# Optimization experiments

Hardware: AMD Instinct MI355X
Metric: run time of the kernel (lower is better)

The kernel has to match this reference:

```python
import jax, jax.numpy as jnp
import numpy as np

N_NODES = 50000
N_EDGES = 400000
IN_C, HID, EDGE_D = 128, 256, 32
NUM_LAYERS = 3

def _gnblock(x, src, dst, edge_attr, ew, eb, nw, nb):
    # edge message MLP: relu(W [x_src, x_dst, e] + b)  -> [E, HID]
    m = jax.nn.relu(jnp.concatenate([x[src], x[dst], edge_attr], axis=-1) @ ew + eb)
    # mean aggregation by destination node
    agg = jax.ops.segment_sum(m, dst, num_segments=N_NODES)
    deg = jax.ops.segment_sum(jnp.ones((m.shape[0],), m.dtype), dst, num_segments=N_NODES)
    agg = agg / jnp.maximum(deg, 1.0)[:, None]
    # node update MLP: relu(W [x, agg] + b) -> [N, HID]
    return jax.nn.relu(jnp.concatenate([x, agg], axis=-1) @ nw + nb)

def setup_inputs() -> dict:
    key = jax.random.key(0)
    ks = jax.random.split(key, 12)
    s = 0.05  # keep activations sane
    return {
        'x': jax.random.normal(ks[0], (N_NODES, IN_C), jnp.float32),
        'edge_index': jax.random.randint(ks[1], (2, N_EDGES), 0, N_NODES, jnp.int32),
        'edge_attr': jax.random.normal(ks[2], (N_EDGES, EDGE_D), jnp.float32),
        'e0_w': jax.random.normal(ks[3], (2 * IN_C + EDGE_D, HID), jnp.float32) * s,
        'e0_b': jnp.zeros((HID,), jnp.float32),
        'n0_w': jax.random.normal(ks[4], (IN_C + HID, HID), jnp.float32) * s,
        'n0_b': jnp.zeros((HID,), jnp.float32),
        'e_w': jax.random.normal(ks[5], (NUM_LAYERS - 1, 2 * HID + EDGE_D, HID), jnp.float32) * s,
        'e_b': jnp.zeros((NUM_LAYERS - 1, HID), jnp.float32),
        'n_w': jax.random.normal(ks[6], (NUM_LAYERS - 1, 2 * HID, HID), jnp.float32) * s,
        'n_b': jnp.zeros((NUM_LAYERS - 1, HID), jnp.float32),
        'h1_w': jax.random.normal(ks[7], (HID, HID), jnp.float32) * s,
        'h1_b': jnp.zeros((HID,), jnp.float32),
        'h2_w': jax.random.normal(ks[8], (HID, 1), jnp.float32) * s,
        'h2_b': jnp.zeros((1,), jnp.float32),
    }

def reference(x, edge_index, edge_attr, e0_w, e0_b, n0_w, n0_b,
              e_w, e_b, n_w, n_b, h1_w, h1_b, h2_w, h2_b):
    src, dst = edge_index[0], edge_index[1]
    h = _gnblock(x, src, dst, edge_attr, e0_w, e0_b, n0_w, n0_b)
    for i in range(NUM_LAYERS - 1):
        h = _gnblock(h, src, dst, edge_attr, e_w[i], e_b[i], n_w[i], n_b[i])
    # MLP head -> per-node logit [N, 1]
    h = jax.nn.relu(h @ h1_w + h1_b)
    return h @ h2_w + h2_b
```

## Files before the change

### kernel.cpp

```cpp
#include <hip/hip_runtime.h>
#include <hip/hip_bf16.h>
#include <hip/hip_fp16.h>

#define NN 50000
#define NE 400000
#define NBLK 196

typedef unsigned short u16;
typedef unsigned int u32;
typedef __attribute__((ext_vector_type(8))) short short8;
typedef __attribute__((ext_vector_type(4))) float f32x4;
typedef __attribute__((ext_vector_type(4))) unsigned short u16x4;
typedef __attribute__((ext_vector_type(2))) _Float16 h2;

typedef __attribute__((address_space(1))) const void as1_void;
typedef __attribute__((address_space(3))) void as3_void;

static __device__ __forceinline__ float bf2f(u16 u) {
    return __uint_as_float(((u32)u) << 16);
}
static __device__ __forceinline__ u16 f2bf(float f) {
    u32 x = __float_as_uint(f);
    x += 0x7fffu + ((x >> 16) & 1u);
    return (u16)(x >> 16);
}
static __device__ __forceinline__ u32 packh2(float a, float b) {
    return ((u32)__half_as_ushort(__float2half(b)) << 16) |
           (u32)__half_as_ushort(__float2half(a));
}
static __device__ __forceinline__ float fdot2u(u32 a, u32 b, float c) {
    return __builtin_amdgcn_fdot2(__builtin_bit_cast(h2, a),
                                  __builtin_bit_cast(h2, b), c, false);
}

static __device__ __forceinline__ void gload_lds16(const u16* g, u16* l) {
    __builtin_amdgcn_global_load_lds((as1_void*)g, (as3_void*)l, 16, 0, 0);
}

__global__ __launch_bounds__(256) void gemm_bt(
    const u16* __restrict__ A, int lda,
    const u16* __restrict__ Bt,
    u16* __restrict__ C, int ldc,
    int M, int K,
    const float* __restrict__ bias,
    int relu)
{
    __shared__ u16 As[128 * 32];
    __shared__ u16 Bs[128 * 32];

    const int t = threadIdx.x;
    const int w = t >> 6;
    const int lane = t & 63;
    const int quad = lane >> 4;
    const int l15 = lane & 15;
    const int tile_m = blockIdx.x * 128;
    const int tile_n = blockIdx.y * 128;
    const int wm = (w >> 1) * 64;
    const int wn = (w & 1) * 64;

    f32x4 acc[4][4];
#pragma unroll
    for (int r = 0; r < 4; ++r)
#pragma unroll
        for (int c = 0; c < 4; ++c)
            acc[r][c] = (f32x4){0.f, 0.f, 0.f, 0.f};

    int ar0 = tile_m + (t >> 2);      if (ar0 > M - 1) ar0 = M - 1;
    int ar1 = tile_m + 64 + (t >> 2); if (ar1 > M - 1) ar1 = M - 1;
    const int br0 = tile_n + (t >> 2);
    const int br1 = tile_n + 64 + (t >> 2);
    const int koff = (t & 3) * 8;

    u16* lAs0 = As + w * 512;
    u16* lAs1 = As + 2048 + w * 512;
    u16* lBs0 = Bs + w * 512;
    u16* lBs1 = Bs + 2048 + w * 512;

    const u16* Arow0 = A + (size_t)ar0 * lda + koff;
    const u16* Arow1 = A + (size_t)ar1 * lda + koff;
    const u16* Brow0 = Bt + (size_t)br0 * K + koff;
    const u16* Brow1 = Bt + (size_t)br1 * K + koff;

    for (int k0 = 0; k0 < K; k0 += 32) {
        gload_lds16(Arow0 + k0, lAs0);
        gload_lds16(Arow1 + k0, lAs1);
        gload_lds16(Brow0 + k0, lBs0);
        gload_lds16(Brow1 + k0, lBs1);
        __syncthreads();

        short8 af[4], bfr[4];
#pragma unroll
        for (int r = 0; r < 4; ++r)
            af[r] = *(const short8*)&As[(wm + r * 16 + l15) * 32 + quad * 8];
#pragma unroll
        for (int c = 0; c < 4; ++c)
            bfr[c] = *(const short8*)&Bs[(wn + c * 16 + l15) * 32 + quad * 8];
#pragma unroll
        for (int r = 0; r < 4; ++r)
#pragma unroll
            for (int c = 0; c < 4; ++c)
                acc[r][c] = __builtin_amdgcn_mfma_f32_16x16x32_bf16(af[r], bfr[c], acc[r][c], 0, 0, 0);
        __syncthreads();
    }

#pragma unroll
    for (int r = 0; r < 4; ++r) {
#pragma unroll
        for (int c = 0; c < 4; ++c) {
            const int coln = tile_n + wn + c * 16 + l15;
            const float bv = bias ? bias[coln] : 0.0f;
#pragma unroll
            for (int i = 0; i < 4; ++i) {
                const int row = tile_m + wm + r * 16 + quad * 4 + i;
                if (row < M) {
                    float v = acc[r][c][i] + bv;
                    if (relu) v = fmaxf(v, 0.f);
                    C[(size_t)row * ldc + coln] = f2bf(v);
                }
            }
        }
    }
}

__global__ __launch_bounds__(256) void edge_agg_fused(
    const u16* __restrict__ P,
    const u32* __restrict__ eattr_p32,
    const u32* __restrict__ WePk,
    const int* __restrict__ row_start,
    const int* __restrict__ src_perm,
    const float* __restrict__ inv_deg,
    u16* __restrict__ aggZ)
{
    const int node = (int)((blockIdx.x * 256 + threadIdx.x) >> 6);
    const int lane = threadIdx.x & 63;
    const int l15 = lane & 15;
    const int col = lane * 4;
    if (node >= NN) return;

    uint4 wpk[16];
#pragma unroll
    for (int kp = 0; kp < 16; ++kp)
        wpk[kp] = *(const uint4*)(WePk + kp * 256 + col);

    u16x4 pdv = *(const u16x4*)(P + (size_t)node * 512 + 256 + col);
    f32x4 pb;
    pb[0] = bf2f(pdv[0]);
    pb[1] = bf2f(pdv[1]);
    pb[2] = bf2f(pdv[2]);
    pb[3] = bf2f(pdv[3]);

    f32x4 accv = (f32x4){0.f, 0.f, 0.f, 0.f};
    const int s0r = row_start[node], s1r = row_start[node + 1];

    if (s1r > s0r) {
        const int jlast = s1r - 1;
        int j1 = (s0r + 1 < jlast) ? s0r + 1 : jlast;
        int sa = src_perm[s0r];
        int sb = src_perm[j1];
        u16x4 psa = *(const u16x4*)(P + (size_t)sa * 512 + col);
        u16x4 psb = *(const u16x4*)(P + (size_t)sb * 512 + col);
        u32 eva = eattr_p32[(size_t)s0r * 16 + l15];
        u32 evb = eattr_p32[(size_t)j1 * 16 + l15];

        for (int j = s0r; j < s1r; ++j) {
            int jc = (j + 2 < jlast) ? j + 2 : jlast;
            int sn = src_perm[jc];
            u16x4 psn = *(const u16x4*)(P + (size_t)sn * 512 + col);
            u32 evn = eattr_p32[(size_t)jc * 16 + l15];

            f32x4 q = pb;
#pragma unroll
            for (int kp = 0; kp < 16; ++kp) {
                u32 evk = (u32)__builtin_amdgcn_readlane((int)eva, kp);
                q[0] = fdot2u(evk, wpk[kp].x, q[0]);
                q[1] = fdot2u(evk, wpk[kp].y, q[1]);
                q[2] = fdot2u(evk, wpk[kp].z, q[2]);
                q[3] = fdot2u(evk, wpk[kp].w, q[3]);
            }
            q[0] += bf2f(psa[0]);
            q[1] += bf2f(psa[1]);
            q[2] += bf2f(psa[2]);
            q[3] += bf2f(psa[3]);
            accv[0] += fmaxf(q[0], 0.f);
            accv[1] += fmaxf(q[1], 0.f);
            accv[2] += fmaxf(q[2], 0.f);
            accv[3] += fmaxf(q[3], 0.f);

            psa = psb; eva = evb;
            psb = psn; evb = evn;
        }
    }

    const float idg = inv_deg[node];
    u16x4 o;
    o[0] = f2bf(accv[0] * idg);
    o[1] = f2bf(accv[1] * idg);
    o[2] = f2bf(accv[2] * idg);
    o[3] = f2bf(accv[3] * idg);
    *(u16x4*)(aggZ + (size_t)node * 512 + col) = o;
}

__global__ __launch_bounds__(256) void head_out(
    const u16* __restrict__ h4Z,
    const float* __restrict__ h2w,
    const float* __restrict__ h2b,
    float* __restrict__ out)
{
    const int node = (int)((blockIdx.x * 256 + threadIdx.x) >> 6);
    const int lane = threadIdx.x & 63;
    if (node >= NN) return;
    const int col = lane * 4;
    u16x4 hv = *(const u16x4*)(h4Z + (size_t)node * 512 + col);
    float4 wv = *(const float4*)(h2w + col);
    float s = bf2f(hv[0]) * wv.x + bf2f(hv[1]) * wv.y +
              bf2f(hv[2]) * wv.z + bf2f(hv[3]) * wv.w;
    for (int off = 32; off > 0; off >>= 1)
        s += __shfl_down(s, off, 64);
    if (lane == 0) out[node] = s + h2b[0];
}

__global__ void zero_int(int* p, int n) {
    int i = blockIdx.x * 256 + threadIdx.x;
    if (i < n) p[i] = 0;
}

__global__ void hist_k(const int* __restrict__ ei, int* __restrict__ deg) {
    int e = blockIdx.x * 256 + threadIdx.x;
    if (e < NE) atomicAdd(&deg[ei[NE + e]], 1);
}

__global__ __launch_bounds__(256) void block_sum_k(const int* __restrict__ deg,
                                                   int* __restrict__ bsum) {
    __shared__ int sm[4];
    const int i = blockIdx.x * 256 + threadIdx.x;
    int v = (i < NN) ? deg[i] : 0;
    for (int off = 32; off > 0; off >>= 1)
        v += __shfl_down(v, off, 64);
    const int lane = threadIdx.x & 63;
    const int w = threadIdx.x >> 6;
    if (lane == 0) sm[w] = v;
    __syncthreads();
    if (threadIdx.x == 0)
        bsum[blockIdx.x] = sm[0] + sm[1] + sm[2] + sm[3];
}

__global__ __launch_bounds__(256) void scan_block_k(const int* __restrict__ bsum,
                                                    int* __restrict__ boff,
                                                    int* __restrict__ row_start) {
    __shared__ int sm[256];
    const int tid = threadIdx.x;
    int v = (tid < NBLK) ? bsum[tid] : 0;
    sm[tid] = v;
    __syncthreads();
    for (int o = 1; o < 256; o <<= 1) {
        int tv = (tid >= o) ? sm[tid - o] : 0;
        __syncthreads();
        sm[tid] += tv;
        __syncthreads();
    }
    if (tid < NBLK) boff[tid] = sm[tid] - v;
    if (tid == NBLK - 1) row_start[NN] = sm[tid];
}

__global__ __launch_bounds__(256) void writeback_k(const int* __restrict__ deg,
                                                   const int* __restrict__ boff,
                                                   int* __restrict__ row_start,
                                                   int* __restrict__ cursor,
                                                   float* __restrict__ inv_deg) {
    __shared__ int sm[256];
    const int tid = threadIdx.x;
    const int i = blockIdx.x * 256 + tid;
    int v = (i < NN) ? deg[i] : 0;
    sm[tid] = v;
    __syncthreads();
    for (int o = 1; o < 256; o <<= 1) {
        int tv = (tid >= o) ? sm[tid - o] : 0;
        __syncthreads();
        sm[tid] += tv;
        __syncthreads();
    }
    if (i < NN) {
        const int rs = boff[blockIdx.x] + sm[tid] - v;
        row_start[i] = rs;
        cursor[i]    = rs;
        inv_deg[i]   = 1.0f / fmaxf((float)v, 1.0f);
    }
}

__global__ void scatter_k(const int* __restrict__ ei, const float* __restrict__ eattr,
                          int* __restrict__ cursor, int* __restrict__ src_perm,
                          u32* __restrict__ eattr_p32) {
    int e = blockIdx.x * 256 + threadIdx.x;
    if (e >= NE) return;
    int s = ei[e], d = ei[NE + e];
    int pos = atomicAdd(&cursor[d], 1);
    src_perm[pos] = s;
    const float* sr = eattr + (size_t)e * 32;
    u32* dr = eattr_p32 + (size_t)pos * 16;
#pragma unroll
    for (int j = 0; j < 16; ++j)
        dr[j] = packh2(sr[2 * j], sr[2 * j + 1]);
}

__global__ void bias_build(const float* __restrict__ e0b,
                           const float* __restrict__ eb1,
                           const float* __restrict__ eb2,
                           float* __restrict__ dst) {
    int i = blockIdx.x * 256 + threadIdx.x;
    if (i >= 1536) return;
    int l = i >> 9, c = i & 511;
    const float* s = (l == 0) ? e0b : (l == 1) ? eb1 : eb2;
    dst[i] = (c < 256) ? 0.f : s[c - 256];
}

struct TJob { const float* src; u16* dst; int K; int ksh; int tr; int dstride; };
struct TJobs { TJob j[16]; };

__global__ void transpose_k(TJobs jobs) {
    TJob jb = jobs.j[blockIdx.y];
    int idx = blockIdx.x * 256 + threadIdx.x;
    if (idx >= (jb.K << 8)) return;
    if (jb.tr == 1) {
        int n = idx >> jb.ksh;
        int k = idx & (jb.K - 1);
        jb.dst[n * jb.dstride + k] = f2bf(jb.src[k * 256 + n]);
    } else {
        int kp = idx >> 8;
        int c = idx & 255;
        ((u32*)jb.dst)[idx] = packh2(jb.src[(2 * kp) * 256 + c],
                                     jb.src[(2 * kp + 1) * 256 + c]);
    }
}

__global__ void cvt_x(const float* __restrict__ src, u16* __restrict__ Z) {
    int i = blockIdx.x * 256 + threadIdx.x;
    if (i >= NN * 128) return;
    int n = i >> 7, c = i & 127;
    Z[(size_t)n * 512 + 256 + c] = f2bf(src[i]);
}

extern "C" void kernel_launch(void* const* d_in, const int* in_sizes, int n_in,
                              void* d_out, int out_size, void* d_ws, size_t ws_size,
                              hipStream_t stream) {
    const float* x     = (const float*)d_in[0];
    const int*   ei    = (const int*)d_in[1];
    const float* eattr = (const float*)d_in[2];
    const float* e0_w  = (const float*)d_in[3];
    const float* e0_b  = (const float*)d_in[4];
    const float* n0_w  = (const float*)d_in[5];
    const float* n0_b  = (const float*)d_in[6];
    const float* e_w   = (const float*)d_in[7];
    const float* e_b   = (const float*)d_in[8];
    const float* n_w   = (const float*)d_in[9];
    const float* n_b   = (const float*)d_in[10];
    const float* h1_w  = (const float*)d_in[11];
    const float* h1_b  = (const float*)d_in[12];
    const float* h2_w  = (const float*)d_in[13];
    const float* h2_b  = (const float*)d_in[14];
    float* out = (float*)d_out;
    (void)in_sizes; (void)n_in; (void)out_size; (void)ws_size;

    char* base = (char*)d_ws;
    size_t off = 0;
    auto alloc = [&](size_t nbytes) -> void* {
        void* p = base + off;
        off += (nbytes + 255) & ~(size_t)255;
        return p;
    };

    int*   deg       = (int*)alloc(NN * 4);
    int*   row_start = (int*)alloc((NN + 1) * 4);
    int*   cursor    = (int*)alloc(NN * 4);
    float* invdeg    = (float*)alloc(NN * 4);
    int*   bsum      = (int*)alloc(NBLK * 4);
    int*   boff      = (int*)alloc(NBLK * 4);
    int*   src_perm  = (int*)alloc(NE * 4);
    u32*   eattr_p32 = (u32*)alloc((size_t)NE * 16 * 4);
    u16*   WcatT0    = (u16*)alloc(512 * 128 * 2);
    u16*   WcatT1    = (u16*)alloc(512 * 256 * 2);
    u16*   WcatT2    = (u16*)alloc(512 * 256 * 2);
    u32*   WePk0     = (u32*)alloc(16 * 256 * 4);
    u32*   WePk1     = (u32*)alloc(16 * 256 * 4);
    u32*   WePk2     = (u32*)alloc(16 * 256 * 4);
    u16*   BcatT0    = (u16*)alloc(256 * 384 * 2);
    u16*   BcatT1    = (u16*)alloc(256 * 512 * 2);
    u16*   BcatT2    = (u16*)alloc(256 * 512 * 2);
    u16*   H1T       = (u16*)alloc(256 * 256 * 2);
    float* bias512   = (float*)alloc(3 * 512 * 4);
    u16*   P         = (u16*)alloc((size_t)NN * 512 * 2);
    u16*   Z0        = (u16*)alloc((size_t)NN * 512 * 2);
    u16*   Z1        = (u16*)alloc((size_t)NN * 512 * 2);

    zero_int<<<(NN + 255) / 256, 256, 0, stream>>>(deg, NN);
    hist_k<<<(NE + 255) / 256, 256, 0, stream>>>(ei, deg);
    block_sum_k<<<NBLK, 256, 0, stream>>>(deg, bsum);
    scan_block_k<<<1, 256, 0, stream>>>(bsum, boff, row_start);
    writeback_k<<<NBLK, 256, 0, stream>>>(deg, boff, row_start, cursor, invdeg);
    scatter_k<<<(NE + 255) / 256, 256, 0, stream>>>(ei, eattr, cursor, src_perm, eattr_p32);
    bias_build<<<6, 256, 0, stream>>>(e0_b, e_b, e_b + 256, bias512);

    const float* ew2 = e_w + 544 * 256;
    const float* nw2 = n_w + 512 * 256;

    TJobs tj;
    auto setj = [&](int i, const float* s, void* d, int K, int tr, int dstride) {
        tj.j[i].src = s; tj.j[i].dst = (u16*)d; tj.j[i].K = K; tj.j[i].tr = tr;
        tj.j[i].dstride = dstride;
        tj.j[i].ksh = (K == 256) ? 8 : (K == 128 ? 7 : 5);
    };
    setj(0,  e0_w,             WcatT0,             128, 1, 128);
    setj(1,  e0_w + 128 * 256, WcatT0 + 256 * 128, 128, 1, 128);
    setj(2,  e_w,              WcatT1,             256, 1, 256);
    setj(3,  e_w + 256 * 256,  WcatT1 + 256 * 256, 256, 1, 256);
    setj(4,  ew2,              WcatT2,             256, 1, 256);
    setj(5,  ew2 + 256 * 256,  WcatT2 + 256 * 256, 256, 1, 256);
    setj(6,  n0_w + 128 * 256, BcatT0,             256, 1, 384);
    setj(7,  n0_w,             BcatT0 + 256,       128, 1, 384);
    setj(8,  n_w + 256 * 256,  BcatT1,             256, 1, 512);
    setj(9,  n_w,              BcatT1 + 256,       256, 1, 512);
    setj(10, nw2 + 256 * 256,  BcatT2,             256, 1, 512);
    setj(11, nw2,              BcatT2 + 256,       256, 1, 512);
    setj(12, h1_w,             H1T,                256, 1, 256);
    setj(13, e0_w + 256 * 256, WePk0,              16,  2, 0);
    setj(14, e_w + 512 * 256,  WePk1,              16,  2, 0);
    setj(15, ew2 + 512 * 256,  WePk2,              16,  2, 0);
    transpose_k<<<dim3(256, 16), 256, 0, stream>>>(tj);

    cvt_x<<<(NN * 128 + 255) / 256, 256, 0, stream>>>(x, Z0);

    const int MT = (NN + 127) / 128;
    u16* WcatT[3] = {WcatT0, WcatT1, WcatT2};
    u32* WePk[3]  = {WePk0, WePk1, WePk2};
    u16* BcatT[3] = {BcatT0, BcatT1, BcatT2};
    const float* nbs[3] = {n0_b, n_b, n_b + 256};
    u16* Zin[3]  = {Z0, Z1, Z0};
    u16* Zout[3] = {Z1, Z0, Z1};
    const int kin[3]  = {128, 256, 256};
    const int knode[3] = {384, 512, 512};

    for (int l = 0; l < 3; ++l) {
        gemm_bt<<<dim3(MT, 4), 256, 0, stream>>>(Zin[l] + 256, 512, WcatT[l], P, 512,
                                                 NN, kin[l], bias512 + l * 512, 0);
        edge_agg_fused<<<NN / 4, 256, 0, stream>>>(P, eattr_p32, WePk[l], row_start,
                                                   src_perm, invdeg, Zin[l]);
        gemm_bt<<<dim3(MT, 2), 256, 0, stream>>>(Zin[l], 512, BcatT[l], Zout[l] + 256, 512,
                                                 NN, knode[l], nbs[l], 1);
    }
    gemm_bt<<<dim3(MT, 2), 256, 0, stream>>>(Z1 + 256, 512, H1T, Z1, 512,
                                             NN, 256, h1_b, 1);
    head_out<<<NN / 4, 256, 0, stream>>>(Z1, h2_w, h2_b, out);
}
```

Measured before the change: 870.3 us.

## Split edge aggregation across two waves per node and pad P row stride

```diff
diff --git a/kernel.cpp b/kernel.cpp
--- a/kernel.cpp
+++ b/kernel.cpp
@@ -5,6 +5,7 @@
 #define NN 50000
 #define NE 400000
 #define NBLK 196
+#define PST 544
 
 typedef unsigned short u16;
 typedef unsigned int u32;
@@ -19,10 +20,19 @@
 static __device__ __forceinline__ float bf2f(u16 u) {
     return __uint_as_float(((u32)u) << 16);
 }
+static __device__ __forceinline__ float bf2f_lo(u32 u) {
+    return __uint_as_float(u << 16);
+}
+static __device__ __forceinline__ float bf2f_hi(u32 u) {
+    return __uint_as_float(u & 0xffff0000u);
+}
 static __device__ __forceinline__ u16 f2bf(float f) {
     u32 x = __float_as_uint(f);
     x += 0x7fffu + ((x >> 16) & 1u);
     return (u16)(x >> 16);
+}
+static __device__ __forceinline__ u32 packbf2(float a, float b) {
+    return ((u32)f2bf(b) << 16) | (u32)f2bf(a);
 }
 static __device__ __forceinline__ u32 packh2(float a, float b) {
     return ((u32)__half_as_ushort(__float2half(b)) << 16) |
@@ -131,25 +141,24 @@
     const float* __restrict__ inv_deg,
     u16* __restrict__ aggZ)
 {
-    const int node = (int)((blockIdx.x * 256 + threadIdx.x) >> 6);
+    const int wid = (int)((blockIdx.x * 256 + threadIdx.x) >> 6);
+    const int node = wid >> 1;
+    const int half = wid & 1;
     const int lane = threadIdx.x & 63;
     const int l15 = lane & 15;
-    const int col = lane * 4;
+    const int coff = half * 128 + lane * 2;
     if (node >= NN) return;
 
-    uint4 wpk[16];
+    uint2 wk[16];
 #pragma unroll
     for (int kp = 0; kp < 16; ++kp)
-        wpk[kp] = *(const uint4*)(WePk + kp * 256 + col);
-
-    u16x4 pdv = *(const u16x4*)(P + (size_t)node * 512 + 256 + col);
-    f32x4 pb;
-    pb[0] = bf2f(pdv[0]);
-    pb[1] = bf2f(pdv[1]);
-    pb[2] = bf2f(pdv[2]);
-    pb[3] = bf2f(pdv[3]);
-
-    f32x4 accv = (f32x4){0.f, 0.f, 0.f, 0.f};
+        wk[kp] = *(const uint2*)(WePk + kp * 256 + coff);
+
+    const u32 pdu = *(const u32*)(P + (size_t)node * PST + 256 + coff);
+    const float pb0 = bf2f_lo(pdu);
+    const float pb1 = bf2f_hi(pdu);
+
+    float acc0 = 0.f, acc1 = 0.f;
     const int s0r = row_start[node], s1r = row_start[node + 1];
 
     if (s1r > s0r) {
@@ -157,34 +166,28 @@
         int j1 = (s0r + 1 < jlast) ? s0r + 1 : jlast;
         int sa = src_perm[s0r];
         int sb = src_perm[j1];
-        u16x4 psa = *(const u16x4*)(P + (size_t)sa * 512 + col);
-        u16x4 psb = *(const u16x4*)(P + (size_t)sb * 512 + col);
+        u32 psa = *(const u32*)(P + (size_t)sa * PST + coff);
+        u32 psb = *(const u32*)(P + (size_t)sb * PST + coff);
         u32 eva = eattr_p32[(size_t)s0r * 16 + l15];
         u32 evb = eattr_p32[(size_t)j1 * 16 + l15];
 
         for (int j = s0r; j < s1r; ++j) {
             int jc = (j + 2 < jlast) ? j + 2 : jlast;
             int sn = src_perm[jc];
-            u16x4 psn = *(const u16x4*)(P + (size_t)sn * 512 + col);
+            u32 psn = *(const u32*)(P + (size_t)sn * PST + coff);
             u32 evn = eattr_p32[(size_t)jc * 16 + l15];
 
-            f32x4 q = pb;
+            float q0 = pb0, q1 = pb1;
 #pragma unroll
             for (int kp = 0; kp < 16; ++kp) {
                 u32 evk = (u32)__builtin_amdgcn_readlane((int)eva, kp);
-                q[0] = fdot2u(evk, wpk[kp].x, q[0]);
-                q[1] = fdot2u(evk, wpk[kp].y, q[1]);
-                q[2] = fdot2u(evk, wpk[kp].z, q[2]);
-                q[3] = fdot2u(evk, wpk[kp].w, q[3]);
+                q0 = fdot2u(evk, wk[kp].x, q0);
+                q1 = fdot2u(evk, wk[kp].y, q1);
             }
-            q[0] += bf2f(psa[0]);
-            q[1] += bf2f(psa[1]);
-            q[2] += bf2f(psa[2]);
-            q[3] += bf2f(psa[3]);
-            accv[0] += fmaxf(q[0], 0.f);
-            accv[1] += fmaxf(q[1], 0.f);
-            accv[2] += fmaxf(q[2], 0.f);
-            accv[3] += fmaxf(q[3], 0.f);
+            q0 += bf2f_lo(psa);
+            q1 += bf2f_hi(psa);
+            acc0 += fmaxf(q0, 0.f);
+            acc1 += fmaxf(q1, 0.f);
 
             psa = psb; eva = evb;
             psb = psn; evb = evn;
@@ -192,12 +195,7 @@
     }
 
     const float idg = inv_deg[node];
-    u16x4 o;
-    o[0] = f2bf(accv[0] * idg);
-    o[1] = f2bf(accv[1] * idg);
-    o[2] = f2bf(accv[2] * idg);
-    o[3] = f2bf(accv[3] * idg);
-    *(u16x4*)(aggZ + (size_t)node * 512 + col) = o;
+    *(u32*)(aggZ + (size_t)node * 512 + coff) = packbf2(acc0 * idg, acc1 * idg);
 }
 
 __global__ __launch_bounds__(256) void head_out(
@@ -296,10 +294,15 @@
     int pos = atomicAdd(&cursor[d], 1);
     src_perm[pos] = s;
     const float* sr = eattr + (size_t)e * 32;
-    u32* dr = eattr_p32 + (size_t)pos * 16;
+    u32 pk[16];
 #pragma unroll
     for (int j = 0; j < 16; ++j)
-        dr[j] = packh2(sr[2 * j], sr[2 * j + 1]);
+        pk[j] = packh2(sr[2 * j], sr[2 * j + 1]);
+    uint4* dr = (uint4*)(eattr_p32 + (size_t)pos * 16);
+    dr[0] = (uint4){pk[0], pk[1], pk[2], pk[3]};
+    dr[1] = (uint4){pk[4], pk[5], pk[6], pk[7]};
+    dr[2] = (uint4){pk[8], pk[9], pk[10], pk[11]};
+    dr[3] = (uint4){pk[12], pk[13], pk[14], pk[15]};
 }
 
 __global__ void bias_build(const float* __restrict__ e0b,
@@ -387,7 +390,7 @@
     u16*   BcatT2    = (u16*)alloc(256 * 512 * 2);
     u16*   H1T       = (u16*)alloc(256 * 256 * 2);
     float* bias512   = (float*)alloc(3 * 512 * 4);
-    u16*   P         = (u16*)alloc((size_t)NN * 512 * 2);
+    u16*   P         = (u16*)alloc((size_t)NN * PST * 2);
     u16*   Z0        = (u16*)alloc((size_t)NN * 512 * 2);
     u16*   Z1        = (u16*)alloc((size_t)NN * 512 * 2);
 
@@ -429,20 +432,21 @@
     cvt_x<<<(NN * 128 + 255) / 256, 256, 0, stream>>>(x, Z0);
 
     const int MT = (NN + 127) / 128;
+    const int AGG_BLK = (2 * NN) / 4;
     u16* WcatT[3] = {WcatT0, WcatT1, WcatT2};
     u32* WePk[3]  = {WePk0, WePk1, WePk2};
     u16* BcatT[3] = {BcatT0, BcatT1, BcatT2};
     const float* nbs[3] = {n0_b, n_b, n_b + 256};
     u16* Zin[3]  = {Z0, Z1, Z0};
     u16* Zout[3] = {Z1, Z0, Z1};
-    const int kin[3]  = {128, 256, 256};
+    const int kin[3]   = {128, 256, 256};
     const int knode[3] = {384, 512, 512};
 
     for (int l = 0; l < 3; ++l) {
-        gemm_bt<<<dim3(MT, 4), 256, 0, stream>>>(Zin[l] + 256, 512, WcatT[l], P, 512,
+        gemm_bt<<<dim3(MT, 4), 256, 0, stream>>>(Zin[l] + 256, 512, WcatT[l], P, PST,
                                                  NN, kin[l], bias512 + l * 512, 0);
-        edge_agg_fused<<<NN / 4, 256, 0, stream>>>(P, eattr_p32, WePk[l], row_start,
-                                                   src_perm, invdeg, Zin[l]);
+        edge_agg_fused<<<AGG_BLK, 256, 0, stream>>>(P, eattr_p32, WePk[l], row_start,
+                                                    src_perm, invdeg, Zin[l]);
         gemm_bt<<<dim3(MT, 2), 256, 0, stream>>>(Zin[l], 512, BcatT[l], Zout[l] + 256, 512,
                                                  NN, knode[l], nbs[l], 1);
     }
```

Result: no change. 854.9 us (-1.8%).
